# Performance work log

Measured on AMD Instinct MI355X. Metric: run time of the kernel, lower is better.

The kernel has to match this reference:

```python
import jax, jax.numpy as jnp
import numpy as np

NUM_HEADS = 16


def setup_inputs() -> dict:
    key = jax.random.key(0)
    k = jax.random.split(key, 5)
    b, s, h = 2, 2048, 1024
    scale = 1.0 / np.sqrt(h)
    return {
        "x": jax.random.normal(k[0], (b, s, h), dtype=jnp.float32),
        "W_qkv": jax.random.normal(k[1], (h, 3 * h), dtype=jnp.float32) * scale,
        "b_qkv": jax.random.normal(k[2], (3 * h,), dtype=jnp.float32) * 0.02,
        "W_o": jax.random.normal(k[3], (h, h), dtype=jnp.float32) * scale,
        "b_o": jax.random.normal(k[4], (h,), dtype=jnp.float32) * 0.02,
    }


def _mha_causal(Q, K, V, num_heads):
    b, s, hd = Q.shape
    d_head = hd // num_heads
    # b s (n h) -> b n s h
    _Q = Q.reshape(b, s, num_heads, d_head).transpose(0, 2, 1, 3)
    _K = K.reshape(b, s, num_heads, d_head).transpose(0, 2, 1, 3)
    _V = V.reshape(b, s, num_heads, d_head).transpose(0, 2, 1, 3)
    scores = jnp.einsum('bnqh,bnkh->bnqk', _Q, _K)
    causal = jnp.tril(jnp.ones((s, s), dtype=bool))  # True where allowed
    scores = jnp.where(causal, scores, -jnp.inf) / jnp.sqrt(jnp.float32(d_head))
    A = jax.nn.softmax(scores, axis=-1)
    AV = jnp.einsum('bnqk,bnkh->bnqh', A, _V)
    return AV.transpose(0, 2, 1, 3).reshape(b, s, hd)


def reference(x, W_qkv, b_qkv, W_o, b_o):
    qkv = x @ W_qkv + b_qkv  # [b, s, 3h]
    Q, K, V = jnp.split(qkv, 3, axis=-1)
    attn = _mha_causal(Q, K, V, NUM_HEADS)
    return attn @ W_o + b_o
```

## Files before the change

kernel.cpp:

```cpp
#include <hip/hip_runtime.h>
#include <hip/hip_bf16.h>

typedef unsigned short u16;
typedef __attribute__((ext_vector_type(8))) short short8;
typedef __attribute__((ext_vector_type(4))) float f32x4;
typedef __attribute__((ext_vector_type(16))) float f32x16;
typedef __attribute__((ext_vector_type(4))) float float4v;
typedef __attribute__((ext_vector_type(4))) unsigned int uint4v;
typedef __attribute__((ext_vector_type(2))) unsigned int uint2v;

__device__ __forceinline__ u16 f2bf(float f) {
    union { float f; unsigned u; } x;
    x.f = f;
    unsigned r = x.u + 0x7fffu + ((x.u >> 16) & 1u);
    return (u16)(r >> 16);
}

__device__ __forceinline__ unsigned cvtpk(float lo, float hi) {
    unsigned r;
    asm("v_cvt_pk_bf16_f32 %0, %1, %2" : "=v"(r) : "v"(lo), "v"(hi));
    return r;
}

__device__ __forceinline__ void gload16(const u16* g, u16* l) {
    __builtin_amdgcn_global_load_lds(
        (const __attribute__((address_space(1))) unsigned*)g,
        (__attribute__((address_space(3))) unsigned*)l, 16, 0, 0);
}

#define WAITV(n) asm volatile("s_waitcnt vmcnt(" #n ")" ::: "memory")

__global__ __launch_bounds__(256) void prep(
    const float* __restrict__ x, const float* __restrict__ Wqkv,
    const float* __restrict__ Wo, u16* __restrict__ x_bf,
    u16* __restrict__ wqkvT, u16* __restrict__ woT) {
    int bid = blockIdx.x;
    int t = threadIdx.x;
    if (bid < 2048) {
        int i = bid * 256 + t;
        const float4v* s = (const float4v*)(x + (size_t)i * 8);
        float4v a = s[0], b = s[1];
        uint4v o;
        o[0] = (unsigned)f2bf(a[0]) | ((unsigned)f2bf(a[1]) << 16);
        o[1] = (unsigned)f2bf(a[2]) | ((unsigned)f2bf(a[3]) << 16);
        o[2] = (unsigned)f2bf(b[0]) | ((unsigned)f2bf(b[1]) << 16);
        o[3] = (unsigned)f2bf(b[2]) | ((unsigned)f2bf(b[3]) << 16);
        *(uint4v*)(x_bf + (size_t)i * 8) = o;
        return;
    }
    const float* src;
    u16* dst;
    int C, tid;
    if (bid < 2816) { tid = bid - 2048; src = Wqkv; dst = wqkvT; C = 3072; }
    else            { tid = bid - 2816; src = Wo;   dst = woT;   C = 1024; }
    int tr = (tid & 15) * 64;
    int tc = (tid >> 4) * 64;
    __shared__ __align__(16) u16 tile[64][72];
    int r = t >> 2;
    int c4 = (t & 3) * 16;
    const float4v* sp = (const float4v*)(src + (size_t)(tr + r) * C + tc + c4);
#pragma unroll
    for (int v = 0; v < 4; v++) {
        float4v xv = sp[v];
#pragma unroll
        for (int j = 0; j < 4; j++) tile[r][c4 + v * 4 + j] = f2bf(xv[j]);
    }
    __syncthreads();
    u16* dp = dst + (size_t)(tc + r) * 1024 + tr + c4;
#pragma unroll
    for (int i = 0; i < 16; i++) dp[i] = tile[c4 + i][r];
}

__global__ __launch_bounds__(256) void gemm_qkv(
    const u16* __restrict__ A, const u16* __restrict__ BT,
    const float* __restrict__ bias, u16* __restrict__ qbuf,
    u16* __restrict__ kvp) {
    const int K = 1024;
    __shared__ __align__(16) u16 SMEM[24576];
    int bm = blockIdx.x, bn = blockIdx.y;
    int t = threadIdx.x;
    int lane = t & 63, wave = t >> 6;
    int wr = wave >> 1, wc = wave & 1;
    f32x4 acc[4][4] = {};

    const u16* gA = A + (size_t)(bm * 128) * K;
    const u16* gB = BT + (size_t)(bn * 128) * K;

    auto stage = [&](int buf, int k0) {
#pragma unroll
        for (int i = 0; i < 2; i++) {
            int o = i * 4096 + t * 16;
            int row = o >> 6;
            int cb = (o & 63) ^ (((row >> 1) & 3) << 4);
            gload16(gA + (size_t)row * K + k0 + (cb >> 1),
                    &SMEM[buf * 4096 + i * 2048 + (t & 192) * 8]);
        }
#pragma unroll
        for (int i = 0; i < 2; i++) {
            int o = i * 4096 + t * 16;
            int row = o >> 6;
            int cb = (o & 63) ^ (((row >> 1) & 3) << 4);
            gload16(gB + (size_t)row * K + k0 + (cb >> 1),
                    &SMEM[12288 + buf * 4096 + i * 2048 + (t & 192) * 8]);
        }
    };

    stage(0, 0);
    stage(1, 32);
    WAITV(4);
    __builtin_amdgcn_s_barrier();

    for (int tt = 0; tt < 32; tt++) {
        bool pre = (tt + 2 < 32);
        if (pre) stage((tt + 2) % 3, (tt + 2) << 5);
        int row16 = lane & 15;
        int colb = ((lane >> 4) * 16) ^ (((row16 >> 1) & 3) << 4);
        const u16* Ab = &SMEM[(tt % 3) * 4096];
        const u16* Bb = &SMEM[12288 + (tt % 3) * 4096];
        short8 af[4], bf[4];
#pragma unroll
        for (int m = 0; m < 4; m++)
            af[m] = *(const short8*)&Ab[(wr * 64 + m * 16 + row16) * 32 + (colb >> 1)];
#pragma unroll
        for (int n = 0; n < 4; n++)
            bf[n] = *(const short8*)&Bb[(wc * 64 + n * 16 + row16) * 32 + (colb >> 1)];
        __builtin_amdgcn_s_setprio(1);
#pragma unroll
        for (int m = 0; m < 4; m++)
#pragma unroll
            for (int n = 0; n < 4; n++)
                acc[m][n] = __builtin_amdgcn_mfma_f32_16x16x32_bf16(
                    af[m], bf[n], acc[m][n], 0, 0, 0);
        __builtin_amdgcn_s_setprio(0);
        if (pre) { WAITV(4); } else { WAITV(0); }
        __builtin_amdgcn_s_barrier();
    }

    int l15 = lane & 15, hi = lane >> 4;
    if (bn < 8) {
#pragma unroll
        for (int m = 0; m < 4; m++)
#pragma unroll
            for (int n = 0; n < 4; n++) {
                int col = bn * 128 + wc * 64 + n * 16 + l15;
                float bv = bias[col];
#pragma unroll
                for (int r = 0; r < 4; r++) {
                    int row = bm * 128 + wr * 64 + m * 16 + hi * 4 + r;
                    qbuf[(size_t)row * 1024 + col] = f2bf(acc[m][n][r] + bv);
                }
            }
    } else if (bn < 16) {
        int h2 = (bn - 8) * 2 + wc;
#pragma unroll
        for (int m = 0; m < 4; m++)
#pragma unroll
            for (int n = 0; n < 4; n++) {
                int d = n * 16 + l15;
                float bv = bias[1024 + h2 * 64 + d];
#pragma unroll
                for (int r = 0; r < 4; r++) {
                    int row = bm * 128 + wr * 64 + m * 16 + hi * 4 + r;
                    int b = row >> 11;
                    int tt = (row & 2047) >> 6;
                    int k = row & 63;
                    kvp[(size_t)(b * 16 + h2) * 262144 + tt * 8192 + k * 64 + d] =
                        f2bf(acc[m][n][r] + bv);
                }
            }
    } else {
        int h2 = (bn - 16) * 2 + wc;
        int rowbase = bm * 128 + wr * 64;
        int b = rowbase >> 11;
        int tt = (rowbase & 2047) >> 6;
        u16* wl = &SMEM[wave * 4608];
#pragma unroll
        for (int m = 0; m < 4; m++)
#pragma unroll
            for (int n = 0; n < 4; n++) {
                int d = n * 16 + l15;
                float bv = bias[2048 + h2 * 64 + d];
                unsigned p0 = cvtpk(acc[m][n][0] + bv, acc[m][n][1] + bv);
                unsigned p1 = cvtpk(acc[m][n][2] + bv, acc[m][n][3] + bv);
                *(uint2v*)&wl[d * 72 + m * 16 + hi * 4] = (uint2v){p0, p1};
            }
        u16* dst = kvp + (size_t)(b * 16 + h2) * 262144 + tt * 8192 + 4096;
#pragma unroll
        for (int i = 0; i < 8; i++)
            *(uint4v*)(dst + lane * 64 + i * 8) = *(const uint4v*)&wl[lane * 72 + i * 8];
    }
}

__global__ __launch_bounds__(256) void gemm_out(
    const u16* __restrict__ A, const u16* __restrict__ BT,
    const float* __restrict__ bias, float* __restrict__ Cout) {
    const int K = 1024, N = 1024;
    __shared__ __align__(16) u16 As[3][4096];
    __shared__ __align__(16) u16 Bs[3][2048];
    int bm = blockIdx.x, bn = blockIdx.y;
    int t = threadIdx.x;
    int lane = t & 63, wave = t >> 6;
    int wr = wave >> 1, wc = wave & 1;
    f32x4 acc[4][2] = {};

    const u16* gA = A + (size_t)(bm * 128) * K;
    const u16* gB = BT + (size_t)(bn * 64) * K;

    auto stage = [&](int buf, int k0) {
#pragma unroll
        for (int i = 0; i < 2; i++) {
            int o = i * 4096 + t * 16;
            int row = o >> 6;
            int cb = (o & 63) ^ (((row >> 1) & 3) << 4);
            gload16(gA + (size_t)row * K + k0 + (cb >> 1),
                    &As[buf][i * 2048 + (t & 192) * 8]);
        }
        {
            int o = t * 16;
            int row = o >> 6;
            int cb = (o & 63) ^ (((row >> 1) & 3) << 4);
            gload16(gB + (size_t)row * K + k0 + (cb >> 1),
                    &Bs[buf][(t & 192) * 8]);
        }
    };

    stage(0, 0);
    stage(1, 32);
    WAITV(3);
    __builtin_amdgcn_s_barrier();

    for (int tt = 0; tt < 32; tt++) {
        bool pre = (tt + 2 < 32);
        if (pre) stage((tt + 2) % 3, (tt + 2) << 5);
        int row16 = lane & 15;
        int colb = ((lane >> 4) * 16) ^ (((row16 >> 1) & 3) << 4);
        short8 af[4], bf[2];
#pragma unroll
        for (int m = 0; m < 4; m++)
            af[m] = *(const short8*)&As[tt % 3][(wr * 64 + m * 16 + row16) * 32 + (colb >> 1)];
#pragma unroll
        for (int n = 0; n < 2; n++)
            bf[n] = *(const short8*)&Bs[tt % 3][(wc * 32 + n * 16 + row16) * 32 + (colb >> 1)];
        __builtin_amdgcn_s_setprio(1);
#pragma unroll
        for (int m = 0; m < 4; m++)
#pragma unroll
            for (int n = 0; n < 2; n++)
                acc[m][n] = __builtin_amdgcn_mfma_f32_16x16x32_bf16(
                    af[m], bf[n], acc[m][n], 0, 0, 0);
        __builtin_amdgcn_s_setprio(0);
        if (pre) { WAITV(3); } else { WAITV(0); }
        __builtin_amdgcn_s_barrier();
    }

#pragma unroll
    for (int m = 0; m < 4; m++)
#pragma unroll
        for (int n = 0; n < 2; n++) {
            int col = bn * 64 + wc * 32 + n * 16 + (lane & 15);
            float bv = bias[col];
#pragma unroll
            for (int r = 0; r < 4; r++) {
                int row = bm * 128 + wr * 64 + m * 16 + (lane >> 4) * 4 + r;
                Cout[(size_t)row * N + col] = acc[m][n][r] + bv;
            }
        }
}

__global__ __launch_bounds__(256, 2) void attn_kernel(
    const u16* __restrict__ qbuf, const u16* __restrict__ kvp,
    u16* __restrict__ attn, float* __restrict__ part_o,
    float* __restrict__ part_l) {
    int bid = blockIdx.x;
    int bh = bid & 31;
    int j = 23 - (bid >> 5);
    int sp, tbeg, tend, kc = 0;
    bool partial;
    if (j >= 8) {
        int idx = j - 8;
        sp = 8 + (idx >> 1);
        kc = idx & 1;
        int half = sp + 1;
        partial = true;
        tbeg = kc ? half : 0;
        tend = kc ? 2 * sp + 2 : half;
    } else {
        sp = j;
        partial = false;
        tbeg = 0;
        tend = 2 * sp + 2;
    }
    int b = bh >> 4, h = bh & 15;
    int t = threadIdx.x;
    int lane = t & 63, w = t >> 6;
    int qb = sp * 128 + w * 32;
    int kend = qb + 32;
    int l31 = lane & 31, hi32 = lane >> 5;
    int swz = (lane & 7) << 4;

    __shared__ __align__(16) u16 KVb[24576];

    const u16* kvb = kvp + (size_t)bh * 262144;

    auto stage = [&](int buf, int tt) {
        const char* g0 = (const char*)(kvb + (size_t)tt * 8192);
#pragma unroll
        for (int kv2 = 0; kv2 < 2; kv2++)
#pragma unroll
            for (int i = 0; i < 2; i++) {
                int o = i * 4096 + t * 16;
                int row = o >> 7;
                int cb = (o & 127) ^ ((row & 7) << 4);
                gload16((const u16*)(g0 + kv2 * 8192 + row * 128 + cb),
                        &KVb[buf * 8192 + kv2 * 4096 + i * 2048 + (t & 192) * 8]);
            }
    };

    short8 qf[4];
    {
        const u16* q0 = qbuf + (size_t)(b * 2048 + qb + l31) * 1024 + h * 64 + hi32 * 8;
#pragma unroll
        for (int dd = 0; dd < 4; dd++) qf[dd] = *(const short8*)(q0 + dd * 16);
    }
    stage(tbeg % 3, tbeg);
    stage((tbeg + 1) % 3, tbeg + 1);

    float l_lane = 0.f;
    f32x16 oT[2] = {};

    const float C1 = 0.1803368880f;
    const float C2 = -17.3123404907f;

    WAITV(4);
    __builtin_amdgcn_s_barrier();

    for (int tt = tbeg; tt < tend; tt++) {
        bool pre = (tt + 2 < tend);
        if (pre) stage((tt + 2) % 3, tt + 2);
        int k0 = tt * 64;
        if (k0 < kend) {
            const u16* Ks = &KVb[(tt % 3) * 8192];
            const u16* Vs = Ks + 4096;
            f32x16 sc[2];
            __builtin_amdgcn_s_setprio(1);
#pragma unroll
            for (int kb = 0; kb < 2; kb++) {
                f32x16 z = {};
#pragma unroll
                for (int dd = 0; dd < 4; dd++) {
                    int off = (kb * 32 + l31) * 64 + (((dd * 32 + hi32 * 16) ^ swz) >> 1);
                    short8 kf = *(const short8*)&Ks[off];
                    z = __builtin_amdgcn_mfma_f32_32x32x16_bf16(kf, qf[dd], z, 0, 0, 0);
                }
                sc[kb] = z;
            }
            __builtin_amdgcn_s_setprio(0);

            float p[2][16];
            int q_g = qb + l31;
            if (k0 + 64 > qb) {
#pragma unroll
                for (int kb = 0; kb < 2; kb++)
#pragma unroll
                    for (int r = 0; r < 16; r++) {
                        int kg = k0 + kb * 32 + (r & 3) + 8 * (r >> 2) + 4 * hi32;
                        float v = (kg <= q_g) ? sc[kb][r] : -1e30f;
                        float pe = __builtin_amdgcn_exp2f(fmaf(v, C1, C2));
                        p[kb][r] = pe;
                        l_lane += pe;
                    }
            } else {
#pragma unroll
                for (int kb = 0; kb < 2; kb++)
#pragma unroll
                    for (int r = 0; r < 16; r++) {
                        float pe = __builtin_amdgcn_exp2f(fmaf(sc[kb][r], C1, C2));
                        p[kb][r] = pe;
                        l_lane += pe;
                    }
            }

            short8 pb[4];
#pragma unroll
            for (int kb = 0; kb < 2; kb++)
#pragma unroll
                for (int cset = 0; cset < 2; cset++) {
                    const float* pp = &p[kb][cset * 8];
                    unsigned A0 = cvtpk(pp[0], pp[1]);
                    unsigned A1 = cvtpk(pp[2], pp[3]);
                    unsigned A2 = cvtpk(pp[4], pp[5]);
                    unsigned A3 = cvtpk(pp[6], pp[7]);
                    unsigned za = hi32 ? A0 : A2;
                    unsigned zb = hi32 ? A1 : A3;
                    unsigned sa = (unsigned)__shfl_xor((int)za, 32, 64);
                    unsigned sb = (unsigned)__shfl_xor((int)zb, 32, 64);
                    uint4v wv;
                    wv[0] = hi32 ? sa : A0;
                    wv[1] = hi32 ? sb : A1;
                    wv[2] = hi32 ? A2 : sa;
                    wv[3] = hi32 ? A3 : sb;
                    pb[kb * 2 + cset] = __builtin_bit_cast(short8, wv);
                }

            __builtin_amdgcn_s_setprio(1);
#pragma unroll
            for (int mb = 0; mb < 2; mb++)
#pragma unroll
                for (int kk = 0; kk < 4; kk++) {
                    int off = (mb * 32 + l31) * 64 + (((kk * 32 + hi32 * 16) ^ swz) >> 1);
                    short8 vf = *(const short8*)&Vs[off];
                    oT[mb] = __builtin_amdgcn_mfma_f32_32x32x16_bf16(vf, pb[kk], oT[mb], 0, 0, 0);
                }
            __builtin_amdgcn_s_setprio(0);
        }
        if (pre) { WAITV(4); } else { WAITV(0); }
        __builtin_amdgcn_s_barrier();
    }

    if (partial) {
        int blk = (bh * 8 + (sp - 8)) * 2 + kc;
        float* po = part_o + (size_t)blk * 8192;
        int lr = w * 32 + l31;
        float lf = l_lane + __shfl_xor(l_lane, 32, 64);
        if (hi32 == 0) part_l[blk * 128 + lr] = lf;
#pragma unroll
        for (int mb = 0; mb < 2; mb++)
#pragma unroll
            for (int r = 0; r < 16; r++) {
                int d = mb * 32 + (r & 3) + 8 * (r >> 2) + 4 * hi32;
                po[lr * 64 + d] = oT[mb][r];
            }
        return;
    }

    float lf = l_lane + __shfl_xor(l_lane, 32, 64);
    float linv = __builtin_amdgcn_rcpf(lf);
    u16* gp = attn + (size_t)(b * 2048 + qb + l31) * 1024 + h * 64;
#pragma unroll
    for (int mb = 0; mb < 2; mb++)
#pragma unroll
        for (int g = 0; g < 4; g++) {
            unsigned w0 = cvtpk(oT[mb][4 * g] * linv, oT[mb][4 * g + 1] * linv);
            unsigned w1 = cvtpk(oT[mb][4 * g + 2] * linv, oT[mb][4 * g + 3] * linv);
            int d0 = mb * 32 + g * 8 + hi32 * 4;
            *(uint2v*)(gp + d0) = (uint2v){w0, w1};
        }
}

__global__ __launch_bounds__(256) void attn_merge(
    const float* __restrict__ part_o, const float* __restrict__ part_l,
    u16* __restrict__ attn) {
    int bid = blockIdx.x;
    int bh = bid & 31;
    int sp8 = bid >> 5;
    int sp = sp8 + 8;
    int b = bh >> 4, h = bh & 15;
    int t = threadIdx.x;
    int blk0 = (bh * 8 + sp8) * 2;
    const float* o0 = part_o + (size_t)blk0 * 8192;
    const float* o1 = o0 + 8192;
    const float* l0 = part_l + blk0 * 128;
    const float* l1 = l0 + 128;
#pragma unroll
    for (int i = 0; i < 4; i++) {
        int r = (t >> 3) + i * 32;
        int d0 = (t & 7) * 8;
        float linv = __builtin_amdgcn_rcpf(l0[r] + l1[r]);
        const float* a = o0 + r * 64 + d0;
        const float* c = o1 + r * 64 + d0;
        uint4v w;
#pragma unroll
        for (int k = 0; k < 4; k++)
            w[k] = cvtpk((a[2 * k] + c[2 * k]) * linv,
                         (a[2 * k + 1] + c[2 * k + 1]) * linv);
        u16* gp = attn + (size_t)(b * 2048 + sp * 128 + r) * 1024 + h * 64 + d0;
        *(uint4v*)gp = w;
    }
}

extern "C" void kernel_launch(void* const* d_in, const int* in_sizes, int n_in,
                              void* d_out, int out_size, void* d_ws, size_t ws_size,
                              hipStream_t stream) {
    const float* x    = (const float*)d_in[0];
    const float* Wqkv = (const float*)d_in[1];
    const float* bqkv = (const float*)d_in[2];
    const float* Wo   = (const float*)d_in[3];
    const float* bo   = (const float*)d_in[4];
    float* out = (float*)d_out;

    char* ws = (char*)d_ws;
    u16* x_bf   = (u16*)(ws);
    u16* attnb  = (u16*)(ws);
    u16* wqkvT  = (u16*)(ws + (8ull << 20));
    u16* woT    = (u16*)(ws + (14ull << 20));
    u16* qbuf   = (u16*)(ws + (16ull << 20));
    u16* kvp    = (u16*)(ws + (24ull << 20));
    float* part_o = (float*)(ws + (40ull << 20));
    float* part_l = (float*)(ws + (56ull << 20));

    prep<<<3072, 256, 0, stream>>>(x, Wqkv, Wo, x_bf, wqkvT, woT);
    gemm_qkv<<<dim3(32, 24), 256, 0, stream>>>(x_bf, wqkvT, bqkv, qbuf, kvp);
    attn_kernel<<<768, 256, 0, stream>>>(qbuf, kvp, attnb, part_o, part_l);
    attn_merge<<<256, 256, 0, stream>>>(part_o, part_l, attnb);
    gemm_out<<<dim3(32, 16), 256, 0, stream>>>(attnb, woT, bo, out);
}
```

Before: 109.3 us.

## Enlarge QKV GEMM tile to 256x256 with 8 waves per block

The QKV projection GEMM moves from 128x128 tiles with 4 waves to 256x256 tiles with 8 waves of 512 threads, each wave now computing a 128x64 sub-tile. Staging, shared-memory buffers and all three epilogues (Q, K and the transposed V write) are reworked for the new tile geometry. The aim is more reuse of each loaded operand and less global/LDS traffic per FLOP. In exchange it doubles LDS and accumulator registers per block and cuts the grid from 768 to 192 blocks, which may underfill the 256 CUs.

```diff
diff --git a/kernel.cpp b/kernel.cpp
--- a/kernel.cpp
+++ b/kernel.cpp
@@ -71,62 +71,63 @@
     for (int i = 0; i < 16; i++) dp[i] = tile[c4 + i][r];
 }
 
-__global__ __launch_bounds__(256) void gemm_qkv(
+__global__ __launch_bounds__(512) void gemm_qkv(
     const u16* __restrict__ A, const u16* __restrict__ BT,
     const float* __restrict__ bias, u16* __restrict__ qbuf,
     u16* __restrict__ kvp) {
     const int K = 1024;
-    __shared__ __align__(16) u16 SMEM[24576];
+    __shared__ __align__(16) u16 SMEM[49152];
     int bm = blockIdx.x, bn = blockIdx.y;
     int t = threadIdx.x;
     int lane = t & 63, wave = t >> 6;
-    int wr = wave >> 1, wc = wave & 1;
-    f32x4 acc[4][4] = {};
-
-    const u16* gA = A + (size_t)(bm * 128) * K;
-    const u16* gB = BT + (size_t)(bn * 128) * K;
-
-    auto stage = [&](int buf, int k0) {
+    int wr = wave >> 2, wc = wave & 3;
+    f32x4 acc[8][4] = {};
+
+    const u16* gA = A + (size_t)(bm * 256) * K;
+    const u16* gB = BT + (size_t)(bn * 256) * K;
+
+    auto stage = [&](int buf, int kt) {
+        int k0 = kt * 32;
 #pragma unroll
         for (int i = 0; i < 2; i++) {
-            int o = i * 4096 + t * 16;
+            int o = i * 8192 + t * 16;
             int row = o >> 6;
             int cb = (o & 63) ^ (((row >> 1) & 3) << 4);
             gload16(gA + (size_t)row * K + k0 + (cb >> 1),
-                    &SMEM[buf * 4096 + i * 2048 + (t & 192) * 8]);
+                    &SMEM[buf * 8192 + i * 4096 + wave * 512]);
         }
 #pragma unroll
         for (int i = 0; i < 2; i++) {
-            int o = i * 4096 + t * 16;
+            int o = i * 8192 + t * 16;
             int row = o >> 6;
             int cb = (o & 63) ^ (((row >> 1) & 3) << 4);
             gload16(gB + (size_t)row * K + k0 + (cb >> 1),
-                    &SMEM[12288 + buf * 4096 + i * 2048 + (t & 192) * 8]);
+                    &SMEM[24576 + buf * 8192 + i * 4096 + wave * 512]);
         }
     };
 
     stage(0, 0);
-    stage(1, 32);
+    stage(1, 1);
     WAITV(4);
     __builtin_amdgcn_s_barrier();
 
-    for (int tt = 0; tt < 32; tt++) {
-        bool pre = (tt + 2 < 32);
-        if (pre) stage((tt + 2) % 3, (tt + 2) << 5);
+    for (int kt = 0; kt < 32; kt++) {
+        bool pre = (kt + 2 < 32);
+        if (pre) stage((kt + 2) % 3, kt + 2);
         int row16 = lane & 15;
         int colb = ((lane >> 4) * 16) ^ (((row16 >> 1) & 3) << 4);
-        const u16* Ab = &SMEM[(tt % 3) * 4096];
-        const u16* Bb = &SMEM[12288 + (tt % 3) * 4096];
-        short8 af[4], bf[4];
-#pragma unroll
-        for (int m = 0; m < 4; m++)
-            af[m] = *(const short8*)&Ab[(wr * 64 + m * 16 + row16) * 32 + (colb >> 1)];
+        const u16* Ab = &SMEM[(kt % 3) * 8192];
+        const u16* Bb = &SMEM[24576 + (kt % 3) * 8192];
+        short8 af[8], bf[4];
+#pragma unroll
+        for (int m = 0; m < 8; m++)
+            af[m] = *(const short8*)&Ab[(wr * 128 + m * 16 + row16) * 32 + (colb >> 1)];
 #pragma unroll
         for (int n = 0; n < 4; n++)
             bf[n] = *(const short8*)&Bb[(wc * 64 + n * 16 + row16) * 32 + (colb >> 1)];
         __builtin_amdgcn_s_setprio(1);
 #pragma unroll
-        for (int m = 0; m < 4; m++)
+        for (int m = 0; m < 8; m++)
 #pragma unroll
             for (int n = 0; n < 4; n++)
                 acc[m][n] = __builtin_amdgcn_mfma_f32_16x16x32_bf16(
@@ -137,57 +138,66 @@
     }
 
     int l15 = lane & 15, hi = lane >> 4;
-    if (bn < 8) {
-#pragma unroll
-        for (int m = 0; m < 4; m++)
+    if (bn < 4) {
+#pragma unroll
+        for (int m = 0; m < 8; m++)
 #pragma unroll
             for (int n = 0; n < 4; n++) {
-                int col = bn * 128 + wc * 64 + n * 16 + l15;
+                int col = bn * 256 + wc * 64 + n * 16 + l15;
                 float bv = bias[col];
 #pragma unroll
-                for (int r = 0; r < 4; r++) {
-                    int row = bm * 128 + wr * 64 + m * 16 + hi * 4 + r;
-                    qbuf[(size_t)row * 1024 + col] = f2bf(acc[m][n][r] + bv);
+                for (int rr = 0; rr < 4; rr++) {
+                    int row = bm * 256 + wr * 128 + m * 16 + hi * 4 + rr;
+                    qbuf[(size_t)row * 1024 + col] = f2bf(acc[m][n][rr] + bv);
                 }
             }
-    } else if (bn < 16) {
-        int h2 = (bn - 8) * 2 + wc;
-#pragma unroll
-        for (int m = 0; m < 4; m++)
+    } else if (bn < 8) {
+        int h2 = (bn - 4) * 4 + wc;
+#pragma unroll
+        for (int m = 0; m < 8; m++)
 #pragma unroll
             for (int n = 0; n < 4; n++) {
                 int d = n * 16 + l15;
                 float bv = bias[1024 + h2 * 64 + d];
 #pragma unroll
-                for (int r = 0; r < 4; r++) {
-                    int row = bm * 128 + wr * 64 + m * 16 + hi * 4 + r;
+                for (int rr = 0; rr < 4; rr++) {
+                    int row = bm * 256 + wr * 128 + m * 16 + hi * 4 + rr;
                     int b = row >> 11;
-                    int tt = (row & 2047) >> 6;
+                    int tv = (row & 2047) >> 6;
                     int k = row & 63;
-                    kvp[(size_t)(b * 16 + h2) * 262144 + tt * 8192 + k * 64 + d] =
-                        f2bf(acc[m][n][r] + bv);
+                    kvp[(size_t)(b * 16 + h2) * 262144 + tv * 8192 + k * 64 + d] =
+                        f2bf(acc[m][n][rr] + bv);
                 }
             }
     } else {
-        int h2 = (bn - 16) * 2 + wc;
-        int rowbase = bm * 128 + wr * 64;
+        int h2 = (bn - 8) * 4 + wc;
+        int rowbase = bm * 256 + wr * 128;
         int b = rowbase >> 11;
-        int tt = (rowbase & 2047) >> 6;
-        u16* wl = &SMEM[wave * 4608];
-#pragma unroll
-        for (int m = 0; m < 4; m++)
-#pragma unroll
-            for (int n = 0; n < 4; n++) {
-                int d = n * 16 + l15;
-                float bv = bias[2048 + h2 * 64 + d];
-                unsigned p0 = cvtpk(acc[m][n][0] + bv, acc[m][n][1] + bv);
-                unsigned p1 = cvtpk(acc[m][n][2] + bv, acc[m][n][3] + bv);
-                *(uint2v*)&wl[d * 72 + m * 16 + hi * 4] = (uint2v){p0, p1};
-            }
-        u16* dst = kvp + (size_t)(b * 16 + h2) * 262144 + tt * 8192 + 4096;
-#pragma unroll
-        for (int i = 0; i < 8; i++)
-            *(uint4v*)(dst + lane * 64 + i * 8) = *(const uint4v*)&wl[lane * 72 + i * 8];
+        int tt0 = (rowbase & 2047) >> 6;
+        u16* wl = &SMEM[wave * 4096];
+#pragma unroll
+        for (int half = 0; half < 2; half++) {
+#pragma unroll
+            for (int nn = 0; nn < 2; nn++) {
+                int n = half * 2 + nn;
+                int dloc = nn * 16 + l15;
+                float bv = bias[2048 + h2 * 64 + n * 16 + l15];
+#pragma unroll
+                for (int m = 0; m < 8; m++) {
+                    unsigned p0 = cvtpk(acc[m][n][0] + bv, acc[m][n][1] + bv);
+                    unsigned p1 = cvtpk(acc[m][n][2] + bv, acc[m][n][3] + bv);
+                    *(uint2v*)&wl[dloc * 128 + m * 16 + hi * 4] = (uint2v){p0, p1};
+                }
+            }
+            int dloc = lane >> 1, seg = lane & 1;
+            int dg = half * 32 + dloc;
+            u16* dst = kvp + (size_t)((b * 16 + h2) * 32 + tt0 + seg) * 8192 +
+                       4096 + dg * 64;
+            const u16* srcp = &wl[dloc * 128 + seg * 64];
+#pragma unroll
+            for (int i = 0; i < 8; i++)
+                *(uint4v*)(dst + i * 8) = *(const uint4v*)(srcp + i * 8);
+        }
     }
 }
 
@@ -499,7 +509,7 @@
     float* part_l = (float*)(ws + (56ull << 20));
 
     prep<<<3072, 256, 0, stream>>>(x, Wqkv, Wo, x_bf, wqkvT, woT);
-    gemm_qkv<<<dim3(32, 24), 256, 0, stream>>>(x_bf, wqkvT, bqkv, qbuf, kvp);
+    gemm_qkv<<<dim3(16, 12), 512, 0, stream>>>(x_bf, wqkvT, bqkv, qbuf, kvp);
     attn_kernel<<<768, 256, 0, stream>>>(qbuf, kvp, attnb, part_o, part_l);
     attn_merge<<<256, 256, 0, stream>>>(part_o, part_l, attnb);
     gemm_out<<<dim3(32, 16), 256, 0, stream>>>(attnb, woT, bo, out);
```

Measured after the change: 111.8 us. 2.3% more time.
